# Kernel optimization log

Measured on AMD Instinct MI355X. Metric: run time of the kernel, lower is better.

## Reference

```python
import jax, jax.numpy as jnp
import numpy as np

CHUNK = 128  # chunk size for the chunked causal linear-attention scan
EPS = 1e-6


def _feature_map(x):
    # elu(x) + 1, matching torch.nn.functional.elu (alpha=1)
    return jax.nn.elu(x) + 1.0


def _causal_linear(Q, K, V):
    """Chunked causal linear attention.

    Q, K: [N, H, L, D], V: [N, H, L, Dv] (float32).
    Computes out[l] = Q[l] @ sum_{s<=l} K[s]^T V[s] without materializing
    the O(L*D*Dv) cumulative outer-product tensor.
    """
    N, H, L, D = Q.shape
    Dv = V.shape[-1]
    C = L // CHUNK
    # [C, N, H, T, D]
    qc = jnp.moveaxis(Q.reshape(N, H, C, CHUNK, D), 2, 0)
    kc = jnp.moveaxis(K.reshape(N, H, C, CHUNK, D), 2, 0)
    vc = jnp.moveaxis(V.reshape(N, H, C, CHUNK, Dv), 2, 0)
    tri = jnp.tril(jnp.ones((CHUNK, CHUNK), dtype=Q.dtype))  # causal mask within chunk

    def step(S, qkv):
        q, k, v = qkv  # [N, H, T, D], [N, H, T, D], [N, H, T, Dv]
        attn = jnp.einsum('nhtd,nhsd->nhts', q, k) * tri
        out = jnp.einsum('nhts,nhse->nhte', attn, v) \
            + jnp.einsum('nhtd,nhde->nhte', q, S)
        S = S + jnp.einsum('nhsd,nhse->nhde', k, v)
        return S, out

    S0 = jnp.zeros((N, H, D, Dv), dtype=Q.dtype)
    _, outs = jax.lax.scan(step, S0, (qc, kc, vc))  # outs: [C, N, H, T, Dv]
    return jnp.moveaxis(outs, 0, 2).reshape(N, H, L, Dv)


def setup_inputs() -> dict:
    key = jax.random.key(0)
    kq, kk, kv = jax.random.split(key, 3)
    shape = (4, 8192, 8, 64)  # [N, L, H, D]
    return {
        'queries': jax.random.normal(kq, shape, dtype=jnp.float32),
        'keys': jax.random.normal(kk, shape, dtype=jnp.float32),
        'values': jax.random.normal(kv, shape, dtype=jnp.float32),
    }


def reference(queries, keys, values):
    dtype = queries.dtype
    Q = _feature_map(queries)  # [N, L, H, D]
    K = _feature_map(keys)
    # normalizer: Z = 1 / (Q . cumsum_l(K) + eps), shape [N, L, H]
    Z = 1.0 / (jnp.einsum('nlhi,nlhi->nlh', Q, jnp.cumsum(K, axis=1)) + EPS)
    # numerator computed in float32 per original causal_linear
    Qf = jnp.transpose(Q, (0, 2, 1, 3)).astype(jnp.float32)
    Kf = jnp.transpose(K, (0, 2, 1, 3)).astype(jnp.float32)
    Vf = jnp.transpose(values, (0, 2, 1, 3)).astype(jnp.float32)
    Vn = _causal_linear(Qf, Kf, Vf)  # [N, H, L, Dv]
    Vn = jnp.transpose(Vn, (0, 2, 1, 3)).astype(dtype)  # [N, L, H, Dv]
    return Vn * Z[:, :, :, None]
```

## Files before the change

kernel.cpp:

```cpp
#include <hip/hip_runtime.h>
#include <math.h>

#define N_    4
#define L_    8192
#define H_    8
#define NH_   32
#define CHK   64
#define NC_   128
#define ROWF  512
#define EPSF  1e-6f

typedef __attribute__((ext_vector_type(8))) short bf16x8;
typedef __attribute__((ext_vector_type(4))) float f32x4;
typedef __attribute__((ext_vector_type(4))) unsigned short us4;

__device__ __forceinline__ float fmap(float x) { return x > 0.f ? x + 1.f : __expf(x); }

__device__ __forceinline__ unsigned short f2bf(float x) {
  unsigned u = __float_as_uint(x);
  u += 0x7FFFu + ((u >> 16) & 1u);
  return (unsigned short)(u >> 16);
}
__device__ __forceinline__ float bf2f(unsigned short u) {
  return __uint_as_float(((unsigned)u) << 16);
}

__device__ __forceinline__ int sidx(int row, int col) {
  return row * 64 + (col ^ ((row & 7) << 3));
}

__device__ __forceinline__ f32x4 MFMA(bf16x8 a, bf16x8 b, f32x4 c) {
  return __builtin_amdgcn_mfma_f32_16x16x32_bf16(a, b, c, 0, 0, 0);
}

__global__ __launch_bounds__(256, 4) void k_chunk_tot(const float* __restrict__ keys,
                                                      const float* __restrict__ values,
                                                      unsigned short* __restrict__ Tws,
                                                      float* __restrict__ Kcs) {
  __shared__ __align__(16) unsigned short Kt[64 * 64];
  __shared__ __align__(16) unsigned short Vt[64 * 64];
  __shared__ float kacc[64];
  const int bid = blockIdx.x;
  const int nh = bid / NC_, c = bid % NC_;
  const int n = nh / H_, h = nh % H_;
  const int tid = threadIdx.x;
  const int lane = tid & 63;
  const int wv = tid >> 6;
  const int lane15 = lane & 15, lg = lane >> 4;
  const int arow = wv * 16 + lane15;

  if (tid < 64) kacc[tid] = 0.f;

  const int d = tid & 63, sg = tid >> 6;
  const size_t gbase = ((size_t)(n * L_ + c * CHK)) * ROWF + h * 64 + d;
  float kr[16], vr[16];
#pragma unroll
  for (int i = 0; i < 16; ++i) {
    const size_t g = gbase + (size_t)(sg * 16 + i) * ROWF;
    kr[i] = keys[g];
    vr[i] = values[g];
  }
  float kpart = 0.f;
#pragma unroll
  for (int i = 0; i < 16; i += 4) {
    us4 wk, wvv;
#pragma unroll
    for (int j = 0; j < 4; ++j) {
      const float kf = fmap(kr[i + j]);
      kpart += kf;
      wk[j] = f2bf(kf);
      wvv[j] = f2bf(vr[i + j]);
    }
    *(us4*)&Kt[sidx(d, sg * 16 + i)] = wk;
    *(us4*)&Vt[sidx(d, sg * 16 + i)] = wvv;
  }
  __syncthreads();

  atomicAdd(&kacc[d], kpart);

  const bf16x8 av0 = *(const bf16x8*)&Vt[sidx(arow, lg * 8)];
  const bf16x8 av1 = *(const bf16x8*)&Vt[sidx(arow, (lg + 4) * 8)];
  us4 tf[4];
#pragma unroll
  for (int nt = 0; nt < 4; ++nt) {
    const int brow = nt * 16 + lane15;
    f32x4 acc = {0.f, 0.f, 0.f, 0.f};
    acc = MFMA(*(const bf16x8*)&Kt[sidx(brow, lg * 8)], av0, acc);
    acc = MFMA(*(const bf16x8*)&Kt[sidx(brow, (lg + 4) * 8)], av1, acc);
#pragma unroll
    for (int r = 0; r < 4; ++r) tf[nt][r] = f2bf(acc[r]);
  }
  __syncthreads();

#pragma unroll
  for (int nt = 0; nt < 4; ++nt)
    *(us4*)&Kt[sidx(arow, nt * 16 + lg * 4)] = tf[nt];
  __syncthreads();

  {
    unsigned short* Tp = Tws + (size_t)bid * 4096;
#pragma unroll
    for (int it = 0; it < 2; ++it) {
      const int i8 = (tid + it * 256) * 8;
      *(uint4*)&Tp[i8] = *(const uint4*)&Kt[i8];
    }
  }
  if (tid < 64) Kcs[(size_t)bid * 64 + tid] = kacc[tid];
}

__global__ __launch_bounds__(256) void k_scan(unsigned short* __restrict__ Tws,
                                              float* __restrict__ Kcs) {
  const int tid = threadIdx.x;
  if (blockIdx.x < 512) {
    const int gid = blockIdx.x * 256 + tid;
    const int nh = gid >> 12, de = gid & 4095;
    unsigned short* p = Tws + (size_t)nh * NC_ * 4096 + de;
    float run = 0.f;
    for (int s = 0; s < 32; ++s) {
      const float x0 = bf2f(p[(size_t)(s * 4 + 0) * 4096]);
      const float x1 = bf2f(p[(size_t)(s * 4 + 1) * 4096]);
      const float x2 = bf2f(p[(size_t)(s * 4 + 2) * 4096]);
      const float x3 = bf2f(p[(size_t)(s * 4 + 3) * 4096]);
      p[(size_t)(s * 4 + 0) * 4096] = f2bf(run);
      p[(size_t)(s * 4 + 1) * 4096] = f2bf(run + x0);
      p[(size_t)(s * 4 + 2) * 4096] = f2bf(run + x0 + x1);
      p[(size_t)(s * 4 + 3) * 4096] = f2bf(run + x0 + x1 + x2);
      run += x0 + x1 + x2 + x3;
    }
  } else {
    const int gid = (blockIdx.x - 512) * 256 + tid;
    const int nh = gid >> 6, d = gid & 63;
    float* p = Kcs + (size_t)nh * NC_ * 64 + d;
    float run = 0.f;
    for (int s = 0; s < 32; ++s) {
      const float x0 = p[(size_t)(s * 4 + 0) * 64];
      const float x1 = p[(size_t)(s * 4 + 1) * 64];
      const float x2 = p[(size_t)(s * 4 + 2) * 64];
      const float x3 = p[(size_t)(s * 4 + 3) * 64];
      p[(size_t)(s * 4 + 0) * 64] = run;
      p[(size_t)(s * 4 + 1) * 64] = run + x0;
      p[(size_t)(s * 4 + 2) * 64] = run + x0 + x1;
      p[(size_t)(s * 4 + 3) * 64] = run + x0 + x1 + x2;
      run += x0 + x1 + x2 + x3;
    }
  }
}

__global__ __launch_bounds__(256, 4) void k_output(const float* __restrict__ queries,
                                                   const float* __restrict__ keys,
                                                   const float* __restrict__ values,
                                                   const unsigned short* __restrict__ Pws,
                                                   const float* __restrict__ Kpre,
                                                   float* __restrict__ out) {
  __shared__ __align__(16) unsigned short Ks[64 * 64];
  __shared__ __align__(16) unsigned short Vt[64 * 64];
  __shared__ __align__(16) unsigned short St[64 * 64];
  __shared__ float kpre[64];

  const int wg = blockIdx.x;
  const int bid = (wg & 7) * (NH_ * NC_ / 8) + (wg >> 3);
  const int nh = bid / NC_, c = bid % NC_;
  const int n = nh / H_, h = nh % H_;
  const int tid = threadIdx.x;
  const int lane = tid & 63;
  const int wv = tid >> 6;
  const int lane15 = lane & 15, lg = lane >> 4;
  const int t0w = wv * 16;
  const int trow = t0w + lane15;
  const int l0 = c * CHK;

  const size_t qg = ((size_t)(n * L_ + l0 + trow)) * ROWF + h * 64;
  const float4 q0 = *(const float4*)&queries[qg + lg * 8];
  const float4 q1 = *(const float4*)&queries[qg + lg * 8 + 4];
  const float4 q2 = *(const float4*)&queries[qg + 32 + lg * 8];
  const float4 q3 = *(const float4*)&queries[qg + 32 + lg * 8 + 4];
  const int r0 = tid >> 4, c4 = (tid & 15) * 4;
  float4 kr[4];
#pragma unroll
  for (int rep = 0; rep < 4; ++rep)
    kr[rep] = *(const float4*)&keys[((size_t)(n * L_ + l0 + r0 + rep * 16)) * ROWF + h * 64 + c4];
  const int d = tid & 63, sg = tid >> 6;
  const size_t vbase = ((size_t)(n * L_ + l0)) * ROWF + h * 64 + d;
  float vr[16];
#pragma unroll
  for (int i = 0; i < 16; ++i) vr[i] = values[vbase + (size_t)(sg * 16 + i) * ROWF];
  const size_t tb = (size_t)bid * 4096;
  const uint4 st0 = *(const uint4*)&Pws[tb + tid * 8];
  const uint4 st1 = *(const uint4*)&Pws[tb + (tid + 256) * 8];
  const float kp = (tid < 64) ? Kpre[(size_t)bid * 64 + tid] : 0.f;

  bf16x8 qf0, qf1;
  qf0[0] = (short)f2bf(fmap(q0.x)); qf0[1] = (short)f2bf(fmap(q0.y));
  qf0[2] = (short)f2bf(fmap(q0.z)); qf0[3] = (short)f2bf(fmap(q0.w));
  qf0[4] = (short)f2bf(fmap(q1.x)); qf0[5] = (short)f2bf(fmap(q1.y));
  qf0[6] = (short)f2bf(fmap(q1.z)); qf0[7] = (short)f2bf(fmap(q1.w));
  qf1[0] = (short)f2bf(fmap(q2.x)); qf1[1] = (short)f2bf(fmap(q2.y));
  qf1[2] = (short)f2bf(fmap(q2.z)); qf1[3] = (short)f2bf(fmap(q2.w));
  qf1[4] = (short)f2bf(fmap(q3.x)); qf1[5] = (short)f2bf(fmap(q3.y));
  qf1[6] = (short)f2bf(fmap(q3.z)); qf1[7] = (short)f2bf(fmap(q3.w));
#pragma unroll
  for (int rep = 0; rep < 4; ++rep) {
    us4 uk;
    uk[0] = f2bf(fmap(kr[rep].x)); uk[1] = f2bf(fmap(kr[rep].y));
    uk[2] = f2bf(fmap(kr[rep].z)); uk[3] = f2bf(fmap(kr[rep].w));
    *(us4*)&Ks[sidx(r0 + rep * 16, c4)] = uk;
  }
#pragma unroll
  for (int i = 0; i < 16; i += 4) {
    us4 w;
#pragma unroll
    for (int j = 0; j < 4; ++j) w[j] = f2bf(vr[i + j]);
    *(us4*)&Vt[sidx(d, sg * 16 + i)] = w;
  }
  *(uint4*)&St[tid * 8] = st0;
  *(uint4*)&St[(tid + 256) * 8] = st1;
  if (tid < 64) kpre[tid] = kp;
  __syncthreads();

  f32x4 aT[4];
#pragma unroll
  for (int nt = 0; nt < 4; ++nt) {
    const int srow = nt * 16 + lane15;
    f32x4 a = {0.f, 0.f, 0.f, 0.f};
    a = MFMA(*(const bf16x8*)&Ks[sidx(srow, lg * 8)], qf0, a);
    a = MFMA(*(const bf16x8*)&Ks[sidx(srow, (lg + 4) * 8)], qf1, a);
    aT[nt] = a;
  }
  float zp = 0.f;
#pragma unroll
  for (int j = 0; j < 8; ++j) zp += bf2f((unsigned short)qf0[j]) * kpre[lg * 8 + j];
#pragma unroll
  for (int j = 0; j < 8; ++j) zp += bf2f((unsigned short)qf1[j]) * kpre[32 + lg * 8 + j];

  __syncthreads();

  float rs = 0.f;
#pragma unroll
  for (int nt = 0; nt < 4; ++nt) {
    us4 w;
#pragma unroll
    for (int r = 0; r < 4; ++r) {
      const int s = nt * 16 + lg * 4 + r;
      const float v = (s <= trow) ? aT[nt][r] : 0.f;
      rs += v;
      w[r] = f2bf(v);
    }
    *(us4*)&Ks[sidx(trow, nt * 16 + lg * 4)] = w;
  }
  float den = rs + zp;
  den += __shfl_xor(den, 16);
  den += __shfl_xor(den, 32);
  const float zv = 1.f / (den + EPSF);

  const bf16x8 af0 = *(const bf16x8*)&Ks[sidx(trow, lg * 8)];
  const bf16x8 af1 = *(const bf16x8*)&Ks[sidx(trow, 32 + lg * 8)];
  const size_t obase = ((size_t)(n * L_ + l0 + trow)) * ROWF + h * 64;
#pragma unroll
  for (int nt = 0; nt < 4; ++nt) {
    const int brow = nt * 16 + lane15;
    f32x4 o = {0.f, 0.f, 0.f, 0.f};
    o = MFMA(*(const bf16x8*)&Vt[sidx(brow, lg * 8)], af0, o);
    o = MFMA(*(const bf16x8*)&Vt[sidx(brow, (lg + 4) * 8)], af1, o);
    o = MFMA(*(const bf16x8*)&St[sidx(brow, lg * 8)], qf0, o);
    o = MFMA(*(const bf16x8*)&St[sidx(brow, (lg + 4) * 8)], qf1, o);
    const float4 w = make_float4(o[0] * zv, o[1] * zv, o[2] * zv, o[3] * zv);
    *(float4*)&out[obase + nt * 16 + lg * 4] = w;
  }
}

extern "C" void kernel_launch(void* const* d_in, const int* in_sizes, int n_in,
                              void* d_out, int out_size, void* d_ws, size_t ws_size,
                              hipStream_t stream) {
  const float* queries = (const float*)d_in[0];
  const float* keys    = (const float*)d_in[1];
  const float* values  = (const float*)d_in[2];
  float* out = (float*)d_out;

  const size_t t_elems = (size_t)NH_ * NC_ * 4096;
  const size_t k_elems = (size_t)NH_ * NC_ * 64;
  if (ws_size < t_elems * 2 + k_elems * 4) return;
  unsigned short* Tws = (unsigned short*)d_ws;
  float* Kcs = (float*)(Tws + t_elems);

  hipLaunchKernelGGL(k_chunk_tot, dim3(NH_ * NC_), dim3(256), 0, stream, keys, values, Tws, Kcs);
  hipLaunchKernelGGL(k_scan, dim3(512 + 8), dim3(256), 0, stream, Tws, Kcs);
  hipLaunchKernelGGL(k_output, dim3(NH_ * NC_), dim3(256), 0, stream,
                     queries, keys, values, Tws, Kcs, out);
}
```

Before: 92.46 us.

## Load prefix state directly into MFMA fragments and drop LDS staging

The chunk kernel now writes its bf16 T tile straight from the MFMA accumulators to global memory, instead of bouncing it through LDS with two extra barriers. The output kernel loads the prefix state S directly from global into per-lane MFMA operand registers and reads the K prefix sums as float4 vectors, which removes the St/kpre shared buffers and a barrier. Other edits switch bf16 conversion to the library intrinsic, compute the normaliser from fp32 features, and drop the occupancy hint from the launch bounds. The cost is more registers per thread and less coalesced global access for the direct fragment loads and stores.

```diff
diff --git a/kernel.cpp b/kernel.cpp
--- a/kernel.cpp
+++ b/kernel.cpp
@@ -1,4 +1,5 @@
 #include <hip/hip_runtime.h>
+#include <hip/hip_bf16.h>
 #include <math.h>
 
 #define N_    4
@@ -16,10 +17,9 @@
 
 __device__ __forceinline__ float fmap(float x) { return x > 0.f ? x + 1.f : __expf(x); }
 
-__device__ __forceinline__ unsigned short f2bf(float x) {
-  unsigned u = __float_as_uint(x);
-  u += 0x7FFFu + ((u >> 16) & 1u);
-  return (unsigned short)(u >> 16);
+__device__ __forceinline__ unsigned short c2bf(float x) {
+  __hip_bfloat16 b = __float2bfloat16(x);
+  return *reinterpret_cast<unsigned short*>(&b);
 }
 __device__ __forceinline__ float bf2f(unsigned short u) {
   return __uint_as_float(((unsigned)u) << 16);
@@ -33,10 +33,10 @@
   return __builtin_amdgcn_mfma_f32_16x16x32_bf16(a, b, c, 0, 0, 0);
 }
 
-__global__ __launch_bounds__(256, 4) void k_chunk_tot(const float* __restrict__ keys,
-                                                      const float* __restrict__ values,
-                                                      unsigned short* __restrict__ Tws,
-                                                      float* __restrict__ Kcs) {
+__global__ __launch_bounds__(256) void k_chunk_tot(const float* __restrict__ keys,
+                                                   const float* __restrict__ values,
+                                                   unsigned short* __restrict__ Tws,
+                                                   float* __restrict__ Kcs) {
   __shared__ __align__(16) unsigned short Kt[64 * 64];
   __shared__ __align__(16) unsigned short Vt[64 * 64];
   __shared__ float kacc[64];
@@ -55,55 +55,37 @@
   const size_t gbase = ((size_t)(n * L_ + c * CHK)) * ROWF + h * 64 + d;
   float kr[16], vr[16];
 #pragma unroll
-  for (int i = 0; i < 16; ++i) {
-    const size_t g = gbase + (size_t)(sg * 16 + i) * ROWF;
-    kr[i] = keys[g];
-    vr[i] = values[g];
-  }
+  for (int i = 0; i < 16; ++i) kr[i] = keys[gbase + (size_t)(sg * 16 + i) * ROWF];
+#pragma unroll
+  for (int i = 0; i < 16; ++i) vr[i] = values[gbase + (size_t)(sg * 16 + i) * ROWF];
+
   float kpart = 0.f;
+#pragma unroll
+  for (int i = 0; i < 16; ++i) { kr[i] = fmap(kr[i]); kpart += kr[i]; }
 #pragma unroll
   for (int i = 0; i < 16; i += 4) {
     us4 wk, wvv;
 #pragma unroll
-    for (int j = 0; j < 4; ++j) {
-      const float kf = fmap(kr[i + j]);
-      kpart += kf;
-      wk[j] = f2bf(kf);
-      wvv[j] = f2bf(vr[i + j]);
-    }
+    for (int j = 0; j < 4; ++j) { wk[j] = c2bf(kr[i + j]); wvv[j] = c2bf(vr[i + j]); }
     *(us4*)&Kt[sidx(d, sg * 16 + i)] = wk;
     *(us4*)&Vt[sidx(d, sg * 16 + i)] = wvv;
   }
+  atomicAdd(&kacc[d], kpart);
   __syncthreads();
-
-  atomicAdd(&kacc[d], kpart);
 
   const bf16x8 av0 = *(const bf16x8*)&Vt[sidx(arow, lg * 8)];
   const bf16x8 av1 = *(const bf16x8*)&Vt[sidx(arow, (lg + 4) * 8)];
-  us4 tf[4];
+  unsigned short* Tp = Tws + (size_t)bid * 4096;
 #pragma unroll
   for (int nt = 0; nt < 4; ++nt) {
     const int brow = nt * 16 + lane15;
     f32x4 acc = {0.f, 0.f, 0.f, 0.f};
     acc = MFMA(*(const bf16x8*)&Kt[sidx(brow, lg * 8)], av0, acc);
     acc = MFMA(*(const bf16x8*)&Kt[sidx(brow, (lg + 4) * 8)], av1, acc);
-#pragma unroll
-    for (int r = 0; r < 4; ++r) tf[nt][r] = f2bf(acc[r]);
-  }
-  __syncthreads();
-
-#pragma unroll
-  for (int nt = 0; nt < 4; ++nt)
-    *(us4*)&Kt[sidx(arow, nt * 16 + lg * 4)] = tf[nt];
-  __syncthreads();
-
-  {
-    unsigned short* Tp = Tws + (size_t)bid * 4096;
-#pragma unroll
-    for (int it = 0; it < 2; ++it) {
-      const int i8 = (tid + it * 256) * 8;
-      *(uint4*)&Tp[i8] = *(const uint4*)&Kt[i8];
-    }
+    us4 w;
+#pragma unroll
+    for (int r = 0; r < 4; ++r) w[r] = c2bf(acc[r]);
+    *(us4*)&Tp[arow * 64 + nt * 16 + lg * 4] = w;
   }
   if (tid < 64) Kcs[(size_t)bid * 64 + tid] = kacc[tid];
 }
@@ -121,10 +103,10 @@
       const float x1 = bf2f(p[(size_t)(s * 4 + 1) * 4096]);
       const float x2 = bf2f(p[(size_t)(s * 4 + 2) * 4096]);
       const float x3 = bf2f(p[(size_t)(s * 4 + 3) * 4096]);
-      p[(size_t)(s * 4 + 0) * 4096] = f2bf(run);
-      p[(size_t)(s * 4 + 1) * 4096] = f2bf(run + x0);
-      p[(size_t)(s * 4 + 2) * 4096] = f2bf(run + x0 + x1);
-      p[(size_t)(s * 4 + 3) * 4096] = f2bf(run + x0 + x1 + x2);
+      p[(size_t)(s * 4 + 0) * 4096] = c2bf(run);
+      p[(size_t)(s * 4 + 1) * 4096] = c2bf(run + x0);
+      p[(size_t)(s * 4 + 2) * 4096] = c2bf(run + x0 + x1);
+      p[(size_t)(s * 4 + 3) * 4096] = c2bf(run + x0 + x1 + x2);
       run += x0 + x1 + x2 + x3;
     }
   } else {
@@ -146,16 +128,14 @@
   }
 }
 
-__global__ __launch_bounds__(256, 4) void k_output(const float* __restrict__ queries,
-                                                   const float* __restrict__ keys,
-                                                   const float* __restrict__ values,
-                                                   const unsigned short* __restrict__ Pws,
-                                                   const float* __restrict__ Kpre,
-                                                   float* __restrict__ out) {
+__global__ __launch_bounds__(256) void k_output(const float* __restrict__ queries,
+                                                const float* __restrict__ keys,
+                                                const float* __restrict__ values,
+                                                const unsigned short* __restrict__ Pws,
+                                                const float* __restrict__ Kpre,
+                                                float* __restrict__ out) {
   __shared__ __align__(16) unsigned short Ks[64 * 64];
   __shared__ __align__(16) unsigned short Vt[64 * 64];
-  __shared__ __align__(16) unsigned short St[64 * 64];
-  __shared__ float kpre[64];
 
   const int wg = blockIdx.x;
   const int bid = (wg & 7) * (NH_ * NC_ / 8) + (wg >> 3);
@@ -168,53 +148,67 @@
   const int t0w = wv * 16;
   const int trow = t0w + lane15;
   const int l0 = c * CHK;
-
+  const size_t tb = (size_t)bid * 4096;
+  const size_t kb = (size_t)bid * 64;
+
+  const int r0 = tid >> 4, c4 = (tid & 15) * 4;
+  float4 krow[4];
+#pragma unroll
+  for (int rep = 0; rep < 4; ++rep)
+    krow[rep] = *(const float4*)&keys[((size_t)(n * L_ + l0 + r0 + rep * 16)) * ROWF + h * 64 + c4];
   const size_t qg = ((size_t)(n * L_ + l0 + trow)) * ROWF + h * 64;
   const float4 q0 = *(const float4*)&queries[qg + lg * 8];
   const float4 q1 = *(const float4*)&queries[qg + lg * 8 + 4];
   const float4 q2 = *(const float4*)&queries[qg + 32 + lg * 8];
   const float4 q3 = *(const float4*)&queries[qg + 32 + lg * 8 + 4];
-  const int r0 = tid >> 4, c4 = (tid & 15) * 4;
-  float4 kr[4];
-#pragma unroll
-  for (int rep = 0; rep < 4; ++rep)
-    kr[rep] = *(const float4*)&keys[((size_t)(n * L_ + l0 + r0 + rep * 16)) * ROWF + h * 64 + c4];
   const int d = tid & 63, sg = tid >> 6;
   const size_t vbase = ((size_t)(n * L_ + l0)) * ROWF + h * 64 + d;
   float vr[16];
 #pragma unroll
   for (int i = 0; i < 16; ++i) vr[i] = values[vbase + (size_t)(sg * 16 + i) * ROWF];
-  const size_t tb = (size_t)bid * 4096;
-  const uint4 st0 = *(const uint4*)&Pws[tb + tid * 8];
-  const uint4 st1 = *(const uint4*)&Pws[tb + (tid + 256) * 8];
-  const float kp = (tid < 64) ? Kpre[(size_t)bid * 64 + tid] : 0.f;
-
-  bf16x8 qf0, qf1;
-  qf0[0] = (short)f2bf(fmap(q0.x)); qf0[1] = (short)f2bf(fmap(q0.y));
-  qf0[2] = (short)f2bf(fmap(q0.z)); qf0[3] = (short)f2bf(fmap(q0.w));
-  qf0[4] = (short)f2bf(fmap(q1.x)); qf0[5] = (short)f2bf(fmap(q1.y));
-  qf0[6] = (short)f2bf(fmap(q1.z)); qf0[7] = (short)f2bf(fmap(q1.w));
-  qf1[0] = (short)f2bf(fmap(q2.x)); qf1[1] = (short)f2bf(fmap(q2.y));
-  qf1[2] = (short)f2bf(fmap(q2.z)); qf1[3] = (short)f2bf(fmap(q2.w));
-  qf1[4] = (short)f2bf(fmap(q3.x)); qf1[5] = (short)f2bf(fmap(q3.y));
-  qf1[6] = (short)f2bf(fmap(q3.z)); qf1[7] = (short)f2bf(fmap(q3.w));
+  bf16x8 stf0[4], stf1[4];
+#pragma unroll
+  for (int nt = 0; nt < 4; ++nt) {
+    const int brow = nt * 16 + lane15;
+    stf0[nt] = *(const bf16x8*)&Pws[tb + brow * 64 + lg * 8];
+    stf1[nt] = *(const bf16x8*)&Pws[tb + brow * 64 + 32 + lg * 8];
+  }
+  const float4 kp0 = *(const float4*)&Kpre[kb + lg * 8];
+  const float4 kp1 = *(const float4*)&Kpre[kb + lg * 8 + 4];
+  const float4 kp2 = *(const float4*)&Kpre[kb + 32 + lg * 8];
+  const float4 kp3 = *(const float4*)&Kpre[kb + 32 + lg * 8 + 4];
+
 #pragma unroll
   for (int rep = 0; rep < 4; ++rep) {
     us4 uk;
-    uk[0] = f2bf(fmap(kr[rep].x)); uk[1] = f2bf(fmap(kr[rep].y));
-    uk[2] = f2bf(fmap(kr[rep].z)); uk[3] = f2bf(fmap(kr[rep].w));
+    uk[0] = c2bf(fmap(krow[rep].x)); uk[1] = c2bf(fmap(krow[rep].y));
+    uk[2] = c2bf(fmap(krow[rep].z)); uk[3] = c2bf(fmap(krow[rep].w));
     *(us4*)&Ks[sidx(r0 + rep * 16, c4)] = uk;
   }
 #pragma unroll
   for (int i = 0; i < 16; i += 4) {
     us4 w;
 #pragma unroll
-    for (int j = 0; j < 4; ++j) w[j] = f2bf(vr[i + j]);
+    for (int j = 0; j < 4; ++j) w[j] = c2bf(vr[i + j]);
     *(us4*)&Vt[sidx(d, sg * 16 + i)] = w;
   }
-  *(uint4*)&St[tid * 8] = st0;
-  *(uint4*)&St[(tid + 256) * 8] = st1;
-  if (tid < 64) kpre[tid] = kp;
+  const float4 f0 = make_float4(fmap(q0.x), fmap(q0.y), fmap(q0.z), fmap(q0.w));
+  const float4 f1 = make_float4(fmap(q1.x), fmap(q1.y), fmap(q1.z), fmap(q1.w));
+  const float4 f2 = make_float4(fmap(q2.x), fmap(q2.y), fmap(q2.z), fmap(q2.w));
+  const float4 f3 = make_float4(fmap(q3.x), fmap(q3.y), fmap(q3.z), fmap(q3.w));
+  bf16x8 qf0, qf1;
+  qf0[0] = (short)c2bf(f0.x); qf0[1] = (short)c2bf(f0.y);
+  qf0[2] = (short)c2bf(f0.z); qf0[3] = (short)c2bf(f0.w);
+  qf0[4] = (short)c2bf(f1.x); qf0[5] = (short)c2bf(f1.y);
+  qf0[6] = (short)c2bf(f1.z); qf0[7] = (short)c2bf(f1.w);
+  qf1[0] = (short)c2bf(f2.x); qf1[1] = (short)c2bf(f2.y);
+  qf1[2] = (short)c2bf(f2.z); qf1[3] = (short)c2bf(f2.w);
+  qf1[4] = (short)c2bf(f3.x); qf1[5] = (short)c2bf(f3.y);
+  qf1[6] = (short)c2bf(f3.z); qf1[7] = (short)c2bf(f3.w);
+  float zp = f0.x * kp0.x + f0.y * kp0.y + f0.z * kp0.z + f0.w * kp0.w
+           + f1.x * kp1.x + f1.y * kp1.y + f1.z * kp1.z + f1.w * kp1.w
+           + f2.x * kp2.x + f2.y * kp2.y + f2.z * kp2.z + f2.w * kp2.w
+           + f3.x * kp3.x + f3.y * kp3.y + f3.z * kp3.z + f3.w * kp3.w;
   __syncthreads();
 
   f32x4 aT[4];
@@ -226,12 +220,6 @@
     a = MFMA(*(const bf16x8*)&Ks[sidx(srow, (lg + 4) * 8)], qf1, a);
     aT[nt] = a;
   }
-  float zp = 0.f;
-#pragma unroll
-  for (int j = 0; j < 8; ++j) zp += bf2f((unsigned short)qf0[j]) * kpre[lg * 8 + j];
-#pragma unroll
-  for (int j = 0; j < 8; ++j) zp += bf2f((unsigned short)qf1[j]) * kpre[32 + lg * 8 + j];
-
   __syncthreads();
 
   float rs = 0.f;
@@ -240,10 +228,10 @@
     us4 w;
 #pragma unroll
     for (int r = 0; r < 4; ++r) {
-      const int s = nt * 16 + lg * 4 + r;
-      const float v = (s <= trow) ? aT[nt][r] : 0.f;
+      const int sc = nt * 16 + lg * 4 + r;
+      const float v = (sc <= trow) ? aT[nt][r] : 0.f;
       rs += v;
-      w[r] = f2bf(v);
+      w[r] = c2bf(v);
     }
     *(us4*)&Ks[sidx(trow, nt * 16 + lg * 4)] = w;
   }
@@ -261,8 +249,8 @@
     f32x4 o = {0.f, 0.f, 0.f, 0.f};
     o = MFMA(*(const bf16x8*)&Vt[sidx(brow, lg * 8)], af0, o);
     o = MFMA(*(const bf16x8*)&Vt[sidx(brow, (lg + 4) * 8)], af1, o);
-    o = MFMA(*(const bf16x8*)&St[sidx(brow, lg * 8)], qf0, o);
-    o = MFMA(*(const bf16x8*)&St[sidx(brow, (lg + 4) * 8)], qf1, o);
+    o = MFMA(stf0[nt], qf0, o);
+    o = MFMA(stf1[nt], qf1, o);
     const float4 w = make_float4(o[0] * zv, o[1] * zv, o[2] * zv, o[3] * zv);
     *(float4*)&out[obase + nt * 16 + lg * 4] = w;
   }
```

Result: slower. 98.84 us (+6.9%).
